# Performance work log

Measured on AMD Instinct MI355X. Metric: run time of the kernel, lower is better.

Reference implementation:

```python
import jax, jax.numpy as jnp
import numpy as np

N_NODES = 100000
N_EDGES = 1600000
IN_FEATS = 128
OUT_FEATS = 128
BN_EPS = 1e-5


def setup_inputs() -> dict:
    key = jax.random.key(0)
    k1, k2, k3, k4, k5 = jax.random.split(key, 5)
    node_feats = jax.random.normal(k1, (N_NODES, IN_FEATS), dtype=jnp.float32)
    W = jax.random.normal(k2, (OUT_FEATS, IN_FEATS), dtype=jnp.float32) * 0.05
    b = jax.random.normal(k3, (OUT_FEATS,), dtype=jnp.float32) * 0.05
    gamma = jnp.ones((OUT_FEATS,), dtype=jnp.float32)
    beta = jnp.zeros((OUT_FEATS,), dtype=jnp.float32)
    src = jax.random.randint(k4, (N_EDGES,), 0, N_NODES, dtype=jnp.int32)
    dst = jax.random.randint(k5, (N_EDGES,), 0, N_NODES, dtype=jnp.int32)
    return {"node_feats": node_feats, "W": W, "b": b, "gamma": gamma,
            "beta": beta, "src": src, "dst": dst}


def reference(node_feats, W, b, gamma, beta, src, dst):
    # Linear projection: [N, in] @ [in, out] + [out]
    h = node_feats @ W.T + b
    # copy_u + sum aggregation over edges, plus self-loop contribution
    # (dgl.add_self_loop adds an edge i->i for every node, so each node
    #  receives its own projected feature exactly once in the sum).
    agg = jax.ops.segment_sum(h[src], dst, num_segments=N_NODES) + h
    # BatchNorm1d (training-mode batch statistics over the node dimension)
    mean = jnp.mean(agg, axis=0)
    var = jnp.var(agg, axis=0)
    h = gamma * (agg - mean) * jax.lax.rsqrt(var + BN_EPS) + beta
    # activation (relu); dropout is identity in eval mode
    h = jax.nn.relu(h)
    # residual sum (in_feats == out_feats, so no residual projection)
    h = h + node_feats
    return h
```

## Files before the change

### kernel.cpp

```cpp
#include <hip/hip_runtime.h>

#define N_NODES 100000
#define N_EDGES 1600000
#define F 128
#define BN_EPS 1e-5f
#define NB 391
#define NBP 392
#define CAP 5120
#define EPB 4096
#define FILL_BLOCKS ((N_EDGES + EPB - 1) / EPB)
#define SP_BLOCKS 2048

#define O_STATS   0
#define O_GCUR    1024
#define O_BBASE   2624
#define O_OFF     4224
#define O_CSR     404288
#define O_PART    404288
#define O_HB      6804352
#define O_BINNED  32404416
#define O_AGGB    32404416
#define O_WB      58004416

typedef __attribute__((ext_vector_type(8))) short bf16x8;
typedef __attribute__((ext_vector_type(4))) float f32x4;

__device__ __forceinline__ unsigned short f2bf(float f) {
    union { float f; unsigned u; } v; v.f = f;
    unsigned u = v.u;
    unsigned r = u + 0x7FFFu + ((u >> 16) & 1u);
    return (unsigned short)(r >> 16);
}

__device__ __forceinline__ float4 bf4_to_f4(ushort4 u) {
    union { unsigned u; float f; } a, b, c, d;
    a.u = (unsigned)u.x << 16; b.u = (unsigned)u.y << 16;
    c.u = (unsigned)u.z << 16; d.u = (unsigned)u.w << 16;
    return make_float4(a.f, b.f, c.f, d.f);
}

__global__ __launch_bounds__(256) void convert_w(
    const float* __restrict__ W, unsigned short* __restrict__ Wb)
{
    int i = blockIdx.x * blockDim.x + threadIdx.x;
    Wb[i] = f2bf(W[i]);
}

__global__ __launch_bounds__(256) void init_cur(int* __restrict__ gcur)
{
    int i = blockIdx.x * blockDim.x + threadIdx.x;
    if (i < NB) gcur[i] = i * CAP;
}

__global__ __launch_bounds__(256) void gemm_front(
    const float* __restrict__ X,
    const unsigned short* __restrict__ Wb,
    const float* __restrict__ bias,
    unsigned short* __restrict__ hb)
{
    __shared__ unsigned short hstage[64 * 132];

    const int t   = threadIdx.x;
    const int w   = t >> 6;
    const int l   = t & 63;
    const int l16 = l & 15;
    const int lk  = l >> 4;
    const int row0    = blockIdx.x * 64;
    const int rowbase = row0 + w * 16;

    int arow   = rowbase + l16;
    int arow_c = (arow < N_NODES) ? arow : 0;

    f32x4 acc[8];
#pragma unroll
    for (int nt = 0; nt < 8; nt++) acc[nt] = (f32x4){0.f, 0.f, 0.f, 0.f};

    const float4* Xf4 = (const float4*)X;
    const bf16x8* W8  = (const bf16x8*)Wb;

#pragma unroll
    for (int ks = 0; ks < 4; ks++) {
        float4 f0 = Xf4[(size_t)arow_c * 32 + (ks * 4 + lk) * 2 + 0];
        float4 f1 = Xf4[(size_t)arow_c * 32 + (ks * 4 + lk) * 2 + 1];
        union { short s[8]; bf16x8 v; } ua;
        ua.s[0] = (short)f2bf(f0.x); ua.s[1] = (short)f2bf(f0.y);
        ua.s[2] = (short)f2bf(f0.z); ua.s[3] = (short)f2bf(f0.w);
        ua.s[4] = (short)f2bf(f1.x); ua.s[5] = (short)f2bf(f1.y);
        ua.s[6] = (short)f2bf(f1.z); ua.s[7] = (short)f2bf(f1.w);
#pragma unroll
        for (int nt = 0; nt < 8; nt++) {
            int col = nt * 16 + l16;
            bf16x8 b = W8[(size_t)col * 16 + ks * 4 + lk];
            acc[nt] = __builtin_amdgcn_mfma_f32_16x16x32_bf16(ua.v, b, acc[nt], 0, 0, 0);
        }
    }

    float bv[8];
#pragma unroll
    for (int nt = 0; nt < 8; nt++) bv[nt] = bias[nt * 16 + l16];
#pragma unroll
    for (int r = 0; r < 4; r++) {
        int rl = w * 16 + lk * 4 + r;
#pragma unroll
        for (int nt = 0; nt < 8; nt++)
            hstage[rl * 132 + nt * 16 + l16] = f2bf(acc[nt][r] + bv[nt]);
    }
    __syncthreads();

#pragma unroll
    for (int it = 0; it < 4; it++) {
        int idx   = t + it * 256;
        int row   = idx >> 4;
        int chunk = idx & 15;
        int grow  = row0 + row;
        if (grow < N_NODES) {
            int4 v = *(const int4*)&hstage[row * 132 + chunk * 8];
            *(int4*)&hb[(size_t)grow * F + chunk * 8] = v;
        }
    }
}

__global__ __launch_bounds__(256) void bin_fill(
    const int* __restrict__ src,
    const int* __restrict__ dst,
    int* __restrict__ gcur,
    int* __restrict__ binned)
{
    __shared__ int hcnt[NBP];
    __shared__ int hloc[NBP];
    __shared__ int hbase[NB];
    __shared__ int ls[256];
    __shared__ int stage[EPB];
    __shared__ unsigned short sbkt[EPB];

    const int t  = threadIdx.x;
    const int eb = blockIdx.x * EPB;

    for (int i = t; i < NBP; i += 256) hcnt[i] = 0;
    __syncthreads();

    int v[16]; int bkt[16];
    unsigned valid = 0;
#pragma unroll
    for (int k = 0; k < 4; k++) {
        int base = eb + t * 4 + k * 1024;
        if (base + 3 < N_EDGES) {
            int4 s4 = *(const int4*)&src[base];
            int4 d4 = *(const int4*)&dst[base];
            bkt[k*4+0] = d4.x >> 8; v[k*4+0] = ((d4.x & 255) << 17) | s4.x;
            bkt[k*4+1] = d4.y >> 8; v[k*4+1] = ((d4.y & 255) << 17) | s4.y;
            bkt[k*4+2] = d4.z >> 8; v[k*4+2] = ((d4.z & 255) << 17) | s4.z;
            bkt[k*4+3] = d4.w >> 8; v[k*4+3] = ((d4.w & 255) << 17) | s4.w;
            valid |= 0xFu << (k * 4);
            atomicAdd(&hcnt[bkt[k*4+0]], 1);
            atomicAdd(&hcnt[bkt[k*4+1]], 1);
            atomicAdd(&hcnt[bkt[k*4+2]], 1);
            atomicAdd(&hcnt[bkt[k*4+3]], 1);
        } else {
#pragma unroll
            for (int j = 0; j < 4; j++) {
                int e = base + j;
                if (e < N_EDGES) {
                    int d = dst[e];
                    bkt[k*4+j] = d >> 8;
                    v[k*4+j]   = ((d & 255) << 17) | src[e];
                    valid |= 1u << (k * 4 + j);
                    atomicAdd(&hcnt[bkt[k*4+j]], 1);
                } else { bkt[k*4+j] = 0; v[k*4+j] = 0; }
            }
        }
    }
    __syncthreads();

    int a0 = (2 * t     < NBP) ? hcnt[2 * t]     : 0;
    int a1 = (2 * t + 1 < NBP) ? hcnt[2 * t + 1] : 0;
    ls[t] = a0 + a1;
    __syncthreads();
    for (int d = 1; d < 256; d <<= 1) {
        int u = (t >= d) ? ls[t - d] : 0;
        __syncthreads();
        ls[t] += u;
        __syncthreads();
    }
    int pb = ls[t] - (a0 + a1);
    if (2 * t     < NBP) hloc[2 * t]     = pb;
    if (2 * t + 1 < NBP) hloc[2 * t + 1] = pb + a0;
    __syncthreads();

    for (int i = t; i < NB; i += 256) {
        int c = hcnt[i];
        hbase[i] = c ? atomicAdd(&gcur[i], c) : 0;
    }
    __syncthreads();

    for (int i = t; i < NBP; i += 256) hcnt[i] = hloc[i];
    __syncthreads();

#pragma unroll
    for (int k = 0; k < 16; k++) {
        if (valid & (1u << k)) {
            int p = atomicAdd(&hcnt[bkt[k]], 1);
            stage[p] = v[k];
            sbkt[p]  = (unsigned short)bkt[k];
        }
    }
    __syncthreads();

    int m = min(EPB, N_EDGES - eb);
#pragma unroll
    for (int k = 0; k < 16; k++) {
        int p = t + k * 256;
        if (p < m) {
            int b = sbkt[p];
            binned[hbase[b] + (p - hloc[b])] = stage[p];
        }
    }
}

__global__ __launch_bounds__(512) void bucket_scan(
    const int* __restrict__ gcur,
    int* __restrict__ bbase)
{
    const int t = threadIdx.x;
    __shared__ int ls[512];
    int c = (t < NB) ? (gcur[t] - t * CAP) : 0;
    ls[t] = c;
    __syncthreads();
    for (int d = 1; d < 512; d <<= 1) {
        int u = (t >= d) ? ls[t - d] : 0;
        __syncthreads();
        ls[t] += u;
        __syncthreads();
    }
    if (t < NB) bbase[t] = ls[t] - c;
    if (t == NB - 1) bbase[NB] = ls[t];
}

__global__ __launch_bounds__(256) void csr_build(
    const int* __restrict__ binned,
    const int* __restrict__ gcur,
    const int* __restrict__ bbase,
    int* __restrict__ offsets,
    int* __restrict__ csr_src)
{
    const int b    = blockIdx.x;
    const int t    = threadIdx.x;
    const int rbeg = b * CAP;
    const int rend = gcur[b];
    const int nb0  = b * 256;

    __shared__ int cnt[256];
    __shared__ int ls[256];
    __shared__ int cur[256];
    cnt[t] = 0;
    __syncthreads();

    for (int i = rbeg + t; i < rend; i += 256)
        atomicAdd(&cnt[binned[i] >> 17], 1);
    __syncthreads();

    int v = cnt[t];
    ls[t] = v;
    __syncthreads();
    for (int d = 1; d < 256; d <<= 1) {
        int u = (t >= d) ? ls[t - d] : 0;
        __syncthreads();
        ls[t] += u;
        __syncthreads();
    }
    int ex = bbase[b] + ls[t] - v;
    cur[t] = ex;
    int node = nb0 + t;
    if (node < N_NODES) offsets[node] = ex;
    if (b == NB - 1 && t == 0) offsets[N_NODES] = N_EDGES;
    __syncthreads();

    for (int i = rbeg + t; i < rend; i += 256) {
        int w   = binned[i];
        int pos = atomicAdd(&cur[w >> 17], 1);
        csr_src[pos] = w & 0x1FFFF;
    }
}

__global__ __launch_bounds__(256) void gather_kernel(
    const unsigned short* __restrict__ hb,
    const int* __restrict__ offsets,
    const int* __restrict__ csr_src,
    unsigned short* __restrict__ aggb)
{
    int g    = blockIdx.x * 8 + (threadIdx.x >> 5);
    int lane = threadIdx.x & 31;
    if (g >= N_NODES) return;

    const ushort4* X4 = (const ushort4*)hb;
    float4 acc = bf4_to_f4(X4[(size_t)g * 32 + lane]);

    int beg = offsets[g];
    int end = offsets[g + 1];

    int e = beg;
    for (; e + 7 < end; e += 8) {
        ushort4 u0 = X4[(size_t)csr_src[e]     * 32 + lane];
        ushort4 u1 = X4[(size_t)csr_src[e + 1] * 32 + lane];
        ushort4 u2 = X4[(size_t)csr_src[e + 2] * 32 + lane];
        ushort4 u3 = X4[(size_t)csr_src[e + 3] * 32 + lane];
        ushort4 u4 = X4[(size_t)csr_src[e + 4] * 32 + lane];
        ushort4 u5 = X4[(size_t)csr_src[e + 5] * 32 + lane];
        ushort4 u6 = X4[(size_t)csr_src[e + 6] * 32 + lane];
        ushort4 u7 = X4[(size_t)csr_src[e + 7] * 32 + lane];
        float4 v0 = bf4_to_f4(u0), v1 = bf4_to_f4(u1);
        float4 v2 = bf4_to_f4(u2), v3 = bf4_to_f4(u3);
        float4 v4 = bf4_to_f4(u4), v5 = bf4_to_f4(u5);
        float4 v6 = bf4_to_f4(u6), v7 = bf4_to_f4(u7);
        acc.x += v0.x + v1.x + v2.x + v3.x + v4.x + v5.x + v6.x + v7.x;
        acc.y += v0.y + v1.y + v2.y + v3.y + v4.y + v5.y + v6.y + v7.y;
        acc.z += v0.z + v1.z + v2.z + v3.z + v4.z + v5.z + v6.z + v7.z;
        acc.w += v0.w + v1.w + v2.w + v3.w + v4.w + v5.w + v6.w + v7.w;
    }
    if (e + 3 < end) {
        ushort4 u0 = X4[(size_t)csr_src[e]     * 32 + lane];
        ushort4 u1 = X4[(size_t)csr_src[e + 1] * 32 + lane];
        ushort4 u2 = X4[(size_t)csr_src[e + 2] * 32 + lane];
        ushort4 u3 = X4[(size_t)csr_src[e + 3] * 32 + lane];
        float4 v0 = bf4_to_f4(u0), v1 = bf4_to_f4(u1);
        float4 v2 = bf4_to_f4(u2), v3 = bf4_to_f4(u3);
        acc.x += v0.x + v1.x + v2.x + v3.x;
        acc.y += v0.y + v1.y + v2.y + v3.y;
        acc.z += v0.z + v1.z + v2.z + v3.z;
        acc.w += v0.w + v1.w + v2.w + v3.w;
        e += 4;
    }
    for (; e < end; ++e) {
        float4 v0 = bf4_to_f4(X4[(size_t)csr_src[e] * 32 + lane]);
        acc.x += v0.x; acc.y += v0.y; acc.z += v0.z; acc.w += v0.w;
    }
    ushort4 o;
    o.x = f2bf(acc.x); o.y = f2bf(acc.y); o.z = f2bf(acc.z); o.w = f2bf(acc.w);
    ((ushort4*)aggb)[(size_t)g * 32 + lane] = o;
}

__global__ __launch_bounds__(256) void stats_partial(
    const unsigned short* __restrict__ aggb,
    float* __restrict__ partial)
{
    const int t    = threadIdx.x;
    const int tc   = t & 31;
    const int trow = t >> 5;
    const int c0   = tc * 4;

    float4 sum = make_float4(0.f, 0.f, 0.f, 0.f);
    float4 ss  = make_float4(0.f, 0.f, 0.f, 0.f);
    for (int r = blockIdx.x * 8 + trow; r < N_NODES; r += SP_BLOCKS * 8) {
        float4 v = bf4_to_f4(((const ushort4*)aggb)[(size_t)r * 32 + tc]);
        sum.x += v.x; sum.y += v.y; sum.z += v.z; sum.w += v.w;
        ss.x  += v.x * v.x; ss.y += v.y * v.y; ss.z += v.z * v.z; ss.w += v.w * v.w;
    }

    __shared__ float red[256 * 8];
    float* my = &red[t * 8];
    my[0] = sum.x; my[1] = sum.y; my[2] = sum.z; my[3] = sum.w;
    my[4] = ss.x;  my[5] = ss.y;  my[6] = ss.z;  my[7] = ss.w;
    __syncthreads();

    if (t < 32) {
        float a8[8];
#pragma unroll
        for (int j = 0; j < 8; j++) a8[j] = red[t * 8 + j];
        for (int gg = 1; gg < 8; gg++)
#pragma unroll
            for (int j = 0; j < 8; j++) a8[j] += red[(gg * 32 + t) * 8 + j];
        float* prow = &partial[(size_t)blockIdx.x * 256];
#pragma unroll
        for (int j = 0; j < 4; j++) {
            prow[t * 4 + j]       = a8[j];
            prow[128 + t * 4 + j] = a8[4 + j];
        }
    }
}

__global__ __launch_bounds__(256) void stats_final(
    const float* __restrict__ partial,
    float* __restrict__ stats)
{
    const int t = threadIdx.x;
    float s = 0.f;
    const float* base = &partial[(size_t)blockIdx.x * 64 * 256];
    for (int r = 0; r < 64; r++)
        s += base[r * 256 + t];
    unsafeAtomicAdd(&stats[t], s);
}

__global__ __launch_bounds__(256) void finalize_kernel(
    const float* __restrict__ stats,
    const float* __restrict__ gamma,
    const float* __restrict__ beta,
    const float* __restrict__ x,
    const unsigned short* __restrict__ aggb,
    float* __restrict__ out)
{
    __shared__ float s_scale[128];
    __shared__ float s_shift[128];
    const int t = threadIdx.x;
    if (t < 128) {
        const float inv_n = 1.0f / (float)N_NODES;
        float mean = stats[t] * inv_n;
        float var  = stats[128 + t] * inv_n - mean * mean;
        float sc   = gamma[t] * rsqrtf(var + BN_EPS);
        s_scale[t] = sc;
        s_shift[t] = beta[t] - mean * sc;
    }
    __syncthreads();

    const long long total = (long long)N_NODES * F / 4;
    long long i0 = (long long)blockIdx.x * blockDim.x + t;
    for (long long i = i0; i < total; i += (long long)gridDim.x * blockDim.x) {
        int cb = (int)(i & 31) * 4;
        float4 v  = bf4_to_f4(((const ushort4*)aggb)[i]);
        float4 xf = ((const float4*)x)[i];
        float4 o;
        o.x = fmaxf(v.x * s_scale[cb + 0] + s_shift[cb + 0], 0.f) + xf.x;
        o.y = fmaxf(v.y * s_scale[cb + 1] + s_shift[cb + 1], 0.f) + xf.y;
        o.z = fmaxf(v.z * s_scale[cb + 2] + s_shift[cb + 2], 0.f) + xf.z;
        o.w = fmaxf(v.w * s_scale[cb + 3] + s_shift[cb + 3], 0.f) + xf.w;
        ((float4*)out)[i] = o;
    }
}

extern "C" void kernel_launch(void* const* d_in, const int* in_sizes, int n_in,
                              void* d_out, int out_size, void* d_ws, size_t ws_size,
                              hipStream_t stream) {
    const float* node_feats = (const float*)d_in[0];
    const float* W          = (const float*)d_in[1];
    const float* b          = (const float*)d_in[2];
    const float* gamma      = (const float*)d_in[3];
    const float* beta       = (const float*)d_in[4];
    const int*   src        = (const int*)d_in[5];
    const int*   dst        = (const int*)d_in[6];

    float* out     = (float*)d_out;
    char*  ws      = (char*)d_ws;
    float* stats   = (float*)(ws + O_STATS);
    int*   gcur    = (int*)(ws + O_GCUR);
    int*   bbase   = (int*)(ws + O_BBASE);
    int*   offsets = (int*)(ws + O_OFF);
    int*   csr_src = (int*)(ws + O_CSR);
    float* partial = (float*)(ws + O_PART);
    unsigned short* hb   = (unsigned short*)(ws + O_HB);
    unsigned short* aggb = (unsigned short*)(ws + O_AGGB);
    unsigned short* Wb   = (unsigned short*)(ws + O_WB);
    int*   binned  = (int*)(ws + O_BINNED);

    hipMemsetAsync(d_ws, 0, 1024, stream);

    convert_w<<<64, 256, 0, stream>>>(W, Wb);
    init_cur<<<2, 256, 0, stream>>>(gcur);

    gemm_front<<<(N_NODES + 63) / 64, 256, 0, stream>>>(node_feats, Wb, b, hb);

    bin_fill<<<FILL_BLOCKS, 256, 0, stream>>>(src, dst, gcur, binned);
    bucket_scan<<<1, 512, 0, stream>>>(gcur, bbase);
    csr_build<<<NB, 256, 0, stream>>>(binned, gcur, bbase, offsets, csr_src);

    gather_kernel<<<(N_NODES + 7) / 8, 256, 0, stream>>>(hb, offsets, csr_src, aggb);

    stats_partial<<<SP_BLOCKS, 256, 0, stream>>>(aggb, partial);
    stats_final<<<32, 256, 0, stream>>>(partial, stats);

    finalize_kernel<<<2048, 256, 0, stream>>>(stats, gamma, beta, node_feats, aggb, out);
}
```

Measured before the change: 171.6 us.

## Use persistent work-stealing gather with per-range atomic node counters

The gather kernel becomes persistent: 2048 blocks pull node indices from 16 atomic counters, each covering a contiguous range of 6250 nodes, instead of launching one half-wave per node. This is meant to balance uneven in-degree work and cut block launch overhead. Separately, the W conversion and cursor init kernels are merged into one setup kernel, saving a launch. The cost is one atomic per node, plus a shuffle and a serialized fetch in each half-wave.

```diff
diff --git a/kernel.cpp b/kernel.cpp
--- a/kernel.cpp
+++ b/kernel.cpp
@@ -10,17 +10,21 @@
 #define EPB 4096
 #define FILL_BLOCKS ((N_EDGES + EPB - 1) / EPB)
 #define SP_BLOCKS 2048
+#define GB_BLOCKS 2048
+#define NRANGE 16
+#define RANGE_SZ 6250
 
 #define O_STATS   0
-#define O_GCUR    1024
-#define O_BBASE   2624
-#define O_OFF     4224
-#define O_CSR     404288
-#define O_PART    404288
-#define O_HB      6804352
-#define O_BINNED  32404416
-#define O_AGGB    32404416
-#define O_WB      58004416
+#define O_WCNT    1024
+#define O_GCUR    2048
+#define O_BBASE   3648
+#define O_OFF     5248
+#define O_CSR     405312
+#define O_PART    405312
+#define O_HB      6805312
+#define O_BINNED  32405376
+#define O_AGGB    32405376
+#define O_WB      58005376
 
 typedef __attribute__((ext_vector_type(8))) short bf16x8;
 typedef __attribute__((ext_vector_type(4))) float f32x4;
@@ -39,16 +43,12 @@
     return make_float4(a.f, b.f, c.f, d.f);
 }
 
-__global__ __launch_bounds__(256) void convert_w(
-    const float* __restrict__ W, unsigned short* __restrict__ Wb)
+__global__ __launch_bounds__(256) void setup_kernel(
+    const float* __restrict__ W, unsigned short* __restrict__ Wb,
+    int* __restrict__ gcur)
 {
     int i = blockIdx.x * blockDim.x + threadIdx.x;
-    Wb[i] = f2bf(W[i]);
-}
-
-__global__ __launch_bounds__(256) void init_cur(int* __restrict__ gcur)
-{
-    int i = blockIdx.x * blockDim.x + threadIdx.x;
+    if (i < 128 * 128) Wb[i] = f2bf(W[i]);
     if (i < NB) gcur[i] = i * CAP;
 }
 
@@ -286,57 +286,68 @@
     const unsigned short* __restrict__ hb,
     const int* __restrict__ offsets,
     const int* __restrict__ csr_src,
-    unsigned short* __restrict__ aggb)
-{
-    int g    = blockIdx.x * 8 + (threadIdx.x >> 5);
-    int lane = threadIdx.x & 31;
-    if (g >= N_NODES) return;
+    unsigned short* __restrict__ aggb,
+    int* __restrict__ wcnt)
+{
+    const int lane  = threadIdx.x & 31;
+    const int rid   = blockIdx.x & (NRANGE - 1);
+    const int gbase = rid * RANGE_SZ;
+    int* cnt = &wcnt[rid * 16];
 
     const ushort4* X4 = (const ushort4*)hb;
-    float4 acc = bf4_to_f4(X4[(size_t)g * 32 + lane]);
-
-    int beg = offsets[g];
-    int end = offsets[g + 1];
-
-    int e = beg;
-    for (; e + 7 < end; e += 8) {
-        ushort4 u0 = X4[(size_t)csr_src[e]     * 32 + lane];
-        ushort4 u1 = X4[(size_t)csr_src[e + 1] * 32 + lane];
-        ushort4 u2 = X4[(size_t)csr_src[e + 2] * 32 + lane];
-        ushort4 u3 = X4[(size_t)csr_src[e + 3] * 32 + lane];
-        ushort4 u4 = X4[(size_t)csr_src[e + 4] * 32 + lane];
-        ushort4 u5 = X4[(size_t)csr_src[e + 5] * 32 + lane];
-        ushort4 u6 = X4[(size_t)csr_src[e + 6] * 32 + lane];
-        ushort4 u7 = X4[(size_t)csr_src[e + 7] * 32 + lane];
-        float4 v0 = bf4_to_f4(u0), v1 = bf4_to_f4(u1);
-        float4 v2 = bf4_to_f4(u2), v3 = bf4_to_f4(u3);
-        float4 v4 = bf4_to_f4(u4), v5 = bf4_to_f4(u5);
-        float4 v6 = bf4_to_f4(u6), v7 = bf4_to_f4(u7);
-        acc.x += v0.x + v1.x + v2.x + v3.x + v4.x + v5.x + v6.x + v7.x;
-        acc.y += v0.y + v1.y + v2.y + v3.y + v4.y + v5.y + v6.y + v7.y;
-        acc.z += v0.z + v1.z + v2.z + v3.z + v4.z + v5.z + v6.z + v7.z;
-        acc.w += v0.w + v1.w + v2.w + v3.w + v4.w + v5.w + v6.w + v7.w;
-    }
-    if (e + 3 < end) {
-        ushort4 u0 = X4[(size_t)csr_src[e]     * 32 + lane];
-        ushort4 u1 = X4[(size_t)csr_src[e + 1] * 32 + lane];
-        ushort4 u2 = X4[(size_t)csr_src[e + 2] * 32 + lane];
-        ushort4 u3 = X4[(size_t)csr_src[e + 3] * 32 + lane];
-        float4 v0 = bf4_to_f4(u0), v1 = bf4_to_f4(u1);
-        float4 v2 = bf4_to_f4(u2), v3 = bf4_to_f4(u3);
-        acc.x += v0.x + v1.x + v2.x + v3.x;
-        acc.y += v0.y + v1.y + v2.y + v3.y;
-        acc.z += v0.z + v1.z + v2.z + v3.z;
-        acc.w += v0.w + v1.w + v2.w + v3.w;
-        e += 4;
-    }
-    for (; e < end; ++e) {
-        float4 v0 = bf4_to_f4(X4[(size_t)csr_src[e] * 32 + lane]);
-        acc.x += v0.x; acc.y += v0.y; acc.z += v0.z; acc.w += v0.w;
-    }
-    ushort4 o;
-    o.x = f2bf(acc.x); o.y = f2bf(acc.y); o.z = f2bf(acc.z); o.w = f2bf(acc.w);
-    ((ushort4*)aggb)[(size_t)g * 32 + lane] = o;
+
+    for (;;) {
+        int gl;
+        if (lane == 0) gl = atomicAdd(cnt, 1);
+        gl = __shfl(gl, 0, 32);
+        if (gl >= RANGE_SZ) break;
+        const int g = gbase + gl;
+
+        float4 acc = bf4_to_f4(X4[(size_t)g * 32 + lane]);
+
+        int beg = offsets[g];
+        int end = offsets[g + 1];
+
+        int e = beg;
+        for (; e + 7 < end; e += 8) {
+            ushort4 u0 = X4[(size_t)csr_src[e]     * 32 + lane];
+            ushort4 u1 = X4[(size_t)csr_src[e + 1] * 32 + lane];
+            ushort4 u2 = X4[(size_t)csr_src[e + 2] * 32 + lane];
+            ushort4 u3 = X4[(size_t)csr_src[e + 3] * 32 + lane];
+            ushort4 u4 = X4[(size_t)csr_src[e + 4] * 32 + lane];
+            ushort4 u5 = X4[(size_t)csr_src[e + 5] * 32 + lane];
+            ushort4 u6 = X4[(size_t)csr_src[e + 6] * 32 + lane];
+            ushort4 u7 = X4[(size_t)csr_src[e + 7] * 32 + lane];
+            float4 v0 = bf4_to_f4(u0), v1 = bf4_to_f4(u1);
+            float4 v2 = bf4_to_f4(u2), v3 = bf4_to_f4(u3);
+            float4 v4 = bf4_to_f4(u4), v5 = bf4_to_f4(u5);
+            float4 v6 = bf4_to_f4(u6), v7 = bf4_to_f4(u7);
+            acc.x += v0.x + v1.x + v2.x + v3.x + v4.x + v5.x + v6.x + v7.x;
+            acc.y += v0.y + v1.y + v2.y + v3.y + v4.y + v5.y + v6.y + v7.y;
+            acc.z += v0.z + v1.z + v2.z + v3.z + v4.z + v5.z + v6.z + v7.z;
+            acc.w += v0.w + v1.w + v2.w + v3.w + v4.w + v5.w + v6.w + v7.w;
+        }
+        if (e + 3 < end) {
+            ushort4 u0 = X4[(size_t)csr_src[e]     * 32 + lane];
+            ushort4 u1 = X4[(size_t)csr_src[e + 1] * 32 + lane];
+            ushort4 u2 = X4[(size_t)csr_src[e + 2] * 32 + lane];
+            ushort4 u3 = X4[(size_t)csr_src[e + 3] * 32 + lane];
+            float4 v0 = bf4_to_f4(u0), v1 = bf4_to_f4(u1);
+            float4 v2 = bf4_to_f4(u2), v3 = bf4_to_f4(u3);
+            acc.x += v0.x + v1.x + v2.x + v3.x;
+            acc.y += v0.y + v1.y + v2.y + v3.y;
+            acc.z += v0.z + v1.z + v2.z + v3.z;
+            acc.w += v0.w + v1.w + v2.w + v3.w;
+            e += 4;
+        }
+        for (; e < end; ++e) {
+            float4 v0 = bf4_to_f4(X4[(size_t)csr_src[e] * 32 + lane]);
+            acc.x += v0.x; acc.y += v0.y; acc.z += v0.z; acc.w += v0.w;
+        }
+        ushort4 o;
+        o.x = f2bf(acc.x); o.y = f2bf(acc.y); o.z = f2bf(acc.z); o.w = f2bf(acc.w);
+        ((ushort4*)aggb)[(size_t)g * 32 + lane] = o;
+    }
 }
 
 __global__ __launch_bounds__(256) void stats_partial(
@@ -346,7 +357,6 @@
     const int t    = threadIdx.x;
     const int tc   = t & 31;
     const int trow = t >> 5;
-    const int c0   = tc * 4;
 
     float4 sum = make_float4(0.f, 0.f, 0.f, 0.f);
     float4 ss  = make_float4(0.f, 0.f, 0.f, 0.f);
@@ -440,6 +450,7 @@
     float* out     = (float*)d_out;
     char*  ws      = (char*)d_ws;
     float* stats   = (float*)(ws + O_STATS);
+    int*   wcnt    = (int*)(ws + O_WCNT);
     int*   gcur    = (int*)(ws + O_GCUR);
     int*   bbase   = (int*)(ws + O_BBASE);
     int*   offsets = (int*)(ws + O_OFF);
@@ -450,10 +461,9 @@
     unsigned short* Wb   = (unsigned short*)(ws + O_WB);
     int*   binned  = (int*)(ws + O_BINNED);
 
-    hipMemsetAsync(d_ws, 0, 1024, stream);
-
-    convert_w<<<64, 256, 0, stream>>>(W, Wb);
-    init_cur<<<2, 256, 0, stream>>>(gcur);
+    hipMemsetAsync(d_ws, 0, 2048, stream);
+
+    setup_kernel<<<64, 256, 0, stream>>>(W, Wb, gcur);
 
     gemm_front<<<(N_NODES + 63) / 64, 256, 0, stream>>>(node_feats, Wb, b, hb);
 
@@ -461,7 +471,7 @@
     bucket_scan<<<1, 512, 0, stream>>>(gcur, bbase);
     csr_build<<<NB, 256, 0, stream>>>(binned, gcur, bbase, offsets, csr_src);
 
-    gather_kernel<<<(N_NODES + 7) / 8, 256, 0, stream>>>(hb, offsets, csr_src, aggb);
+    gather_kernel<<<GB_BLOCKS, 256, 0, stream>>>(hb, offsets, csr_src, aggb, wcnt);
 
     stats_partial<<<SP_BLOCKS, 256, 0, stream>>>(aggb, partial);
     stats_final<<<32, 256, 0, stream>>>(partial, stats);
```

New measurement: 215.0 us. 25.3% more time.
